# Optimization experiments

Measured on AMD Instinct MI355X. Metric: run time of the kernel, lower is better.

Reference implementation:

```python
import jax, jax.numpy as jnp
import numpy as np

N = 50000   # nodes
E = 800000  # edges (avg degree 16)
D = 64      # in = hidden = out channels, head = 1


def _linear_params(key, d_in, d_out):
    kw, kb = jax.random.split(key)
    scale = 1.0 / np.sqrt(d_in)
    W = jax.random.uniform(kw, (d_in, d_out), jnp.float32, -scale, scale)
    b = jax.random.uniform(kb, (d_out,), jnp.float32, -scale, scale)
    return W, b


def _tconv(x, src, dst, Wq, bq, Wk, bk, Wv, bv, Ws, bs):
    """PyG TransformerConv, heads=1, concat=True, root_weight=True."""
    n = x.shape[0]
    d = Wq.shape[1]
    q = x @ Wq + bq  # [N, d] query at target
    k = x @ Wk + bk  # [N, d] key at source
    v = x @ Wv + bv  # [N, d] value at source
    # per-edge attention logits: (q_i . k_j) / sqrt(d)
    scores = jnp.einsum('ed,ed->e', q[dst], k[src]) / jnp.sqrt(jnp.asarray(d, x.dtype))
    # segment softmax over incoming edges of each target node
    m = jax.ops.segment_max(scores, dst, num_segments=n)
    ex = jnp.exp(scores - m[dst])
    denom = jax.ops.segment_sum(ex, dst, num_segments=n)
    agg = jax.ops.segment_sum(ex[:, None] * v[src], dst, num_segments=n)
    denom_safe = jnp.where(denom > 0, denom, 1.0)  # guard isolated nodes
    return agg / denom_safe[:, None] + (x @ Ws + bs)  # + skip (root weight)


def setup_inputs() -> dict:
    key = jax.random.key(0)
    keys = jax.random.split(key, 32)
    inp = {
        'x': jax.random.normal(keys[0], (N, D), jnp.float32),
        'edge_index': jax.random.randint(keys[1], (2, E), 0, N, jnp.int64),
        'z': jax.random.normal(keys[2], (N, D), jnp.float32),
    }
    ki = 3
    for l in (1, 2, 3):
        for nm in ('q', 'k', 'v', 's'):
            W, b = _linear_params(keys[ki], D, D)
            ki += 1
            inp[f'W{nm}{l}'] = W
            inp[f'b{nm}{l}'] = b
    return inp


def reference(x, edge_index, z,
              Wq1, bq1, Wk1, bk1, Wv1, bv1, Ws1, bs1,
              Wq2, bq2, Wk2, bk2, Wv2, bv2, Ws2, bs2,
              Wq3, bq3, Wk3, bk3, Wv3, bv3, Ws3, bs3):
    src, dst = edge_index[0], edge_index[1]
    h = jax.nn.silu(_tconv(x, src, dst, Wq1, bq1, Wk1, bk1, Wv1, bv1, Ws1, bs1))
    h = jax.nn.silu(_tconv(h, src, dst, Wq2, bq2, Wk2, bk2, Wv2, bv2, Ws2, bs2) + h)
    drift = _tconv(h, src, dst, Wq3, bq3, Wk3, bk3, Wv3, bv3, Ws3, bs3)
    std, sqrt_d = 0.01, 0.1
    return drift + std * z / sqrt_d
```

## Files before the change

kernel.cpp:

```cpp
#include <hip/hip_runtime.h>
#include <math.h>


#define D64 64
#define KVF 64
#define NPB 128
#define MAXNB 512
#define CHUNK 4096

typedef _Float16 h2 __attribute__((ext_vector_type(2)));
typedef __attribute__((ext_vector_type(8))) short bf16x8;
typedef __attribute__((ext_vector_type(4))) float f32x4;
typedef unsigned int uint32;

__device__ __forceinline__ unsigned short bf16_rne(float f) {
    unsigned int u = __float_as_uint(f);
    u += 0x7FFFu + ((u >> 16) & 1u);
    return (unsigned short)(u >> 16);
}
__device__ __forceinline__ float fexp(float x) {
    return __builtin_amdgcn_exp2f(x * 1.44269504089f);
}
__device__ __forceinline__ float frcp(float x) {
    return __builtin_amdgcn_rcpf(x);
}

__global__ void detect_fmt(const int* __restrict__ ei, int nchecks, int* flag) {
    int t = blockIdx.x * blockDim.x + threadIdx.x;
    int acc = 0;
    for (int i = t; i < nchecks; i += blockDim.x * gridDim.x)
        acc |= ei[2 * i + 1];
    if (acc) atomicOr(flag, 1);
}

__device__ __forceinline__ int load_src(const int* ei, int e, int E, int is64) {
    return is64 ? ei[2 * e] : ei[e];
}
__device__ __forceinline__ int load_dst(const int* ei, int e, int E, int is64) {
    return is64 ? ei[2 * E + 2 * e] : ei[E + e];
}

__global__ void hist_pack(const int* __restrict__ ei, int* __restrict__ bhT,
                          uint32* __restrict__ pc, int E, int nblk, int NB,
                          const int* __restrict__ flag) {
    __shared__ int h[MAXNB];
    int blk = blockIdx.x, tid = threadIdx.x;
    for (int i = tid; i < NB; i += 256) h[i] = 0;
    __syncthreads();
    int is64 = (*flag == 0);
    int e1 = blk * CHUNK + CHUNK; if (e1 > E) e1 = E;
    for (int e = blk * CHUNK + tid; e < e1; e += 256) {
        int s = load_src(ei, e, E, is64);
        int d = load_dst(ei, e, E, is64);
        pc[e] = (uint32)s | ((uint32)d << 16);
        atomicAdd(&h[d >> 7], 1);
    }
    __syncthreads();
    for (int i = tid; i < NB; i += 256) bhT[i * nblk + blk] = h[i];
}

__global__ void scan_blocks(const int* __restrict__ counts, int* __restrict__ partial,
                            int* __restrict__ blockSums, int n) {
    int tid = threadIdx.x;
    int base = blockIdx.x * 1024 + tid * 4;
    int4 c = make_int4(0, 0, 0, 0);
    if (base + 3 < n) c = *(const int4*)&counts[base];
    else {
        if (base + 0 < n) c.x = counts[base + 0];
        if (base + 1 < n) c.y = counts[base + 1];
        if (base + 2 < n) c.z = counts[base + 2];
        if (base + 3 < n) c.w = counts[base + 3];
    }
    int s1 = c.x, s2 = s1 + c.y, s3 = s2 + c.z, s4 = s3 + c.w;
    int lane = tid & 63, wave = tid >> 6;
    int v = s4;
#pragma unroll
    for (int off = 1; off < 64; off <<= 1) {
        int t = __shfl_up(v, off);
        if (lane >= off) v += t;
    }
    __shared__ int wsum[4];
    if (lane == 63) wsum[wave] = v;
    __syncthreads();
    int wpre = 0;
    for (int w = 0; w < wave; ++w) wpre += wsum[w];
    int pre = wpre + v - s4;
    if (base + 0 < n) partial[base + 0] = pre + s1;
    if (base + 1 < n) partial[base + 1] = pre + s2;
    if (base + 2 < n) partial[base + 2] = pre + s3;
    if (base + 3 < n) partial[base + 3] = pre + s4;
    if (tid == 255) blockSums[blockIdx.x] = wsum[0] + wsum[1] + wsum[2] + wsum[3];
}

__global__ void scan_sums(int* __restrict__ bs, int nb) {
    int lane = threadIdx.x;
    int carry = 0;
    for (int b0 = 0; b0 < nb; b0 += 64) {
        int i = b0 + lane;
        int val = (i < nb) ? bs[i] : 0;
        int v = val;
#pragma unroll
        for (int off = 1; off < 64; off <<= 1) {
            int t = __shfl_up(v, off);
            if (lane >= off) v += t;
        }
        if (i < nb) bs[i] = carry + v - val;
        carry += __shfl(v, 63);
    }
}

__global__ void make_excl(const int* __restrict__ bh, const int* __restrict__ partial,
                          const int* __restrict__ bs, int* __restrict__ ebase, int n) {
    int i = blockIdx.x * 256 + threadIdx.x;
    if (i >= n) return;
    ebase[i] = partial[i] + bs[i >> 10] - bh[i];
}

__global__ void bucket_scatter(const uint32* __restrict__ pc, const int* __restrict__ ebase,
                               uint32* __restrict__ pairs, int E, int nblk, int NB) {
    __shared__ int cur[MAXNB];
    int blk = blockIdx.x, tid = threadIdx.x;
    for (int i = tid; i < NB; i += 256) cur[i] = ebase[i * nblk + blk];
    __syncthreads();
    int e1 = blk * CHUNK + CHUNK; if (e1 > E) e1 = E;
    for (int e = blk * CHUNK + tid; e < e1; e += 256) {
        uint32 w = pc[e];
        int pos = atomicAdd(&cur[w >> 23], 1);
        pairs[pos] = w;
    }
}

__global__ void bucket_finalize(const uint32* __restrict__ pairs,
                                const int* __restrict__ ebase, int nblk, int NB,
                                int* __restrict__ csr_src, int* __restrict__ offsets,
                                int N, int E) {
    __shared__ int hist[NPB];
    __shared__ int cur[NPB];
    int b = blockIdx.x, tid = threadIdx.x;
    int n0 = b * NPB;
    int cnt = N - n0; if (cnt > NPB) cnt = NPB;
    if (cnt <= 0) return;
    int estart = ebase[b * nblk];
    int eend = (b + 1 < NB) ? ebase[(b + 1) * nblk] : E;
    for (int i = tid; i < cnt; i += 256) hist[i] = 0;
    __syncthreads();
    for (int e = estart + tid; e < eend; e += 256)
        atomicAdd(&hist[(int)(pairs[e] >> 16) - n0], 1);
    __syncthreads();
    if (tid == 0) {
        int run = estart;
        for (int i = 0; i < cnt; ++i) {
            cur[i] = run;
            offsets[n0 + i] = run;
            run += hist[i];
        }
    }
    if (b == 0 && tid == 1) offsets[N] = E;
    __syncthreads();
    for (int e = estart + tid; e < eend; e += 256) {
        uint32 w = pairs[e];
        int pos = atomicAdd(&cur[(int)(w >> 16) - n0], 1);
        csr_src[pos] = (int)(w & 0xFFFFu);
    }
}

__global__ void prep_w(const float* W0, const float* W1, const float* W2,
                       const float* W3, const float* W4, const float* W5,
                       const float* W6, const float* W7, const float* W8,
                       const float* W9, const float* W10, const float* W11,
                       uint32* __restrict__ wpack) {
    const float* Wm;
    switch (blockIdx.x) {
        case 0: Wm = W0; break;  case 1: Wm = W1; break;
        case 2: Wm = W2; break;  case 3: Wm = W3; break;
        case 4: Wm = W4; break;  case 5: Wm = W5; break;
        case 6: Wm = W6; break;  case 7: Wm = W7; break;
        case 8: Wm = W8; break;  case 9: Wm = W9; break;
        case 10: Wm = W10; break; default: Wm = W11; break;
    }
    int layer = blockIdx.x >> 2, mat = blockIdx.x & 3;
    uint32* hiB = wpack + layer * 16384;
    uint32* loB = hiB + 8192;
    int d = threadIdx.x & 63;
    int cg = threadIdx.x >> 6;
    int col = mat * 64 + d;
    for (int kw = cg; kw < 32; kw += 4) {
        float w0 = Wm[(2 * kw) * 64 + d];
        float w1 = Wm[(2 * kw + 1) * 64 + d];
        unsigned short h0 = bf16_rne(w0);
        unsigned short h1 = bf16_rne(w1);
        float r0 = w0 - __uint_as_float(((uint32)h0) << 16);
        float r1 = w1 - __uint_as_float(((uint32)h1) << 16);
        unsigned short l0 = bf16_rne(r0);
        unsigned short l1 = bf16_rne(r1);
        int sw = ((kw * 4) ^ ((col & 7) << 4)) >> 2;
        hiB[col * 32 + sw] = (uint32)h0 | ((uint32)h1 << 16);
        loB[col * 32 + sw] = (uint32)l0 | ((uint32)l1 << 16);
    }
}

__launch_bounds__(256)
__global__ void gemm_mfma(const float* __restrict__ x, const uint32* __restrict__ wpackL,
                          const float* __restrict__ bq, const float* __restrict__ bk,
                          const float* __restrict__ bv, const float* __restrict__ bs,
                          float* __restrict__ q, float* __restrict__ kv,
                          float* __restrict__ s, int n) {
    __shared__ uint32 wlds[16384];
    int tid = threadIdx.x;
#pragma unroll
    for (int r = 0; r < 16; ++r) {
        int w4 = r * 1024 + tid * 4;
        *(uint4*)&wlds[w4] = *(const uint4*)&wpackL[w4];
    }
    __syncthreads();

    int lane = tid & 63, wave = tid >> 6;
    int row0 = blockIdx.x * 64 + wave * 16;
    int arow = row0 + (lane & 15);
    int kgrp = (lane >> 4) * 8;
    bool rowok = arow < n;
    const float* xr = x + (size_t)(rowok ? arow : 0) * D64;

    bf16x8 ahi[2], alo[2];
#pragma unroll
    for (int st = 0; st < 2; ++st) {
        float4 xa = rowok ? *(const float4*)(xr + st * 32 + kgrp)
                          : make_float4(0.f, 0.f, 0.f, 0.f);
        float4 xb = rowok ? *(const float4*)(xr + st * 32 + kgrp + 4)
                          : make_float4(0.f, 0.f, 0.f, 0.f);
        float xs[8] = {xa.x, xa.y, xa.z, xa.w, xb.x, xb.y, xb.z, xb.w};
#pragma unroll
        for (int j = 0; j < 8; ++j) {
            unsigned short h = bf16_rne(xs[j]);
            float rem = xs[j] - __uint_as_float(((uint32)h) << 16);
            ahi[st][j] = (short)h;
            alo[st][j] = (short)bf16_rne(rem);
        }
    }

    f32x4 acc[16];
#pragma unroll
    for (int t = 0; t < 16; ++t) acc[t] = f32x4{0.f, 0.f, 0.f, 0.f};

#pragma unroll
    for (int t = 0; t < 16; ++t) {
        int col = t * 16 + (lane & 15);
#pragma unroll
        for (int st = 0; st < 2; ++st) {
            int kidx = st * 32 + kgrp;
            int boff = col * 128 + ((kidx * 2) ^ ((col & 7) << 4));
            bf16x8 bhi = *(const bf16x8*)((const char*)wlds + boff);
            bf16x8 blo = *(const bf16x8*)((const char*)wlds + boff + 32768);
            acc[t] = __builtin_amdgcn_mfma_f32_16x16x32_bf16(alo[st], bhi, acc[t], 0, 0, 0);
            acc[t] = __builtin_amdgcn_mfma_f32_16x16x32_bf16(ahi[st], blo, acc[t], 0, 0, 0);
            acc[t] = __builtin_amdgcn_mfma_f32_16x16x32_bf16(ahi[st], bhi, acc[t], 0, 0, 0);
        }
    }

    int drow0 = row0 + (lane >> 4) * 4;
    int c16 = lane & 15;
#pragma unroll
    for (int t = 0; t < 4; ++t) {
        float bb = bq[t * 16 + c16];
#pragma unroll
        for (int r = 0; r < 4; ++r) {
            int row = drow0 + r;
            if (row < n) q[(size_t)row * D64 + t * 16 + c16] = acc[t][r] + bb;
        }
    }
#pragma unroll
    for (int t = 0; t < 4; ++t) {
        float bb = bs[t * 16 + c16];
#pragma unroll
        for (int r = 0; r < 4; ++r) {
            int row = drow0 + r;
            if (row < n) s[(size_t)row * D64 + t * 16 + c16] = acc[12 + t][r] + bb;
        }
    }
#pragma unroll
    for (int t = 0; t < 4; ++t) {
        float bkk = bk[t * 16 + c16];
        float bvv = bv[t * 16 + c16];
        int c = t * 16 + c16;
#pragma unroll
        for (int r = 0; r < 4; ++r) {
            int row = drow0 + r;
            float kval = acc[4 + t][r] + bkk;
            float vval = acc[8 + t][r] + bvv;
            uint32 kh = (uint32)__builtin_bit_cast(unsigned short, (_Float16)kval);
            uint32 kp = (uint32)__shfl_xor((int)kh, 1);
            uint32 kword = (lane & 1) ? (kp | (kh << 16)) : (kh | (kp << 16));
            uint32 vh = (uint32)bf16_rne(vval);
            uint32 vp = (uint32)__shfl_xor((int)vh, 1);
            uint32 vword = (lane & 1) ? (vp | (vh << 16)) : (vh | (vp << 16));
            if (row < n && !(lane & 1)) {
                uint32* rowp = (uint32*)(kv + (size_t)row * KVF);
                rowp[c >> 1] = kword;
                rowp[32 + (c >> 1)] = vword;
            }
        }
    }
}

template <int MODE>
__launch_bounds__(256)
__global__ void agg_fused(const float* __restrict__ q, const float* __restrict__ kv,
                          const int* __restrict__ csr_src,
                          const int* __restrict__ offsets,
                          const float* __restrict__ sbuf, const float* __restrict__ xin,
                          const float* __restrict__ z, float* __restrict__ out, int n) {
    int node = blockIdx.x * 4 + (threadIdx.x >> 6);
    if (node >= n) return;
    int lane = threadIdx.x & 63;
    int grp = lane >> 3, l8 = lane & 7;
    int start = offsets[node], end = offsets[node + 1];
    size_t co = (size_t)node * D64 + l8 * 8;
    float4 ta = *(const float4*)(sbuf + co);
    float4 tb = *(const float4*)(sbuf + co + 4);

    if (end > start) {
        const float4 qa = *(const float4*)(q + co);
        const float4 qb = *(const float4*)(q + co + 4);
        h2 hq0, hq1, hq2, hq3;
        hq0[0] = (_Float16)(qa.x * 0.125f); hq0[1] = (_Float16)(qa.y * 0.125f);
        hq1[0] = (_Float16)(qa.z * 0.125f); hq1[1] = (_Float16)(qa.w * 0.125f);
        hq2[0] = (_Float16)(qb.x * 0.125f); hq2[1] = (_Float16)(qb.y * 0.125f);
        hq3[0] = (_Float16)(qb.z * 0.125f); hq3[1] = (_Float16)(qb.w * 0.125f);
        float m = -3.0e38f, den = 0.f;
        float4 aa = make_float4(0.f, 0.f, 0.f, 0.f);
        float4 ab = make_float4(0.f, 0.f, 0.f, 0.f);

        int i = start + grp;
        int idx0 = (i < end) ? i : start;
        int sj0 = csr_src[idx0];
        const float* kp0 = kv + (size_t)sj0 * KVF;
        float4 kw = *(const float4*)(kp0 + l8 * 4);
        float4 vw = *(const float4*)(kp0 + 32 + l8 * 4);

        while (i < end) {
            int inext = i + 8;
            int idx1 = (inext < end) ? inext : start;
            int sj1 = csr_src[idx1];
            const float* kp1 = kv + (size_t)sj1 * KVF;
            float4 kw1 = *(const float4*)(kp1 + l8 * 4);
            float4 vw1 = *(const float4*)(kp1 + 32 + l8 * 4);

            float p = __builtin_amdgcn_fdot2(hq0, __builtin_bit_cast(h2, kw.x),
                                             0.f, false);
            p = __builtin_amdgcn_fdot2(hq1, __builtin_bit_cast(h2, kw.y), p, false);
            p = __builtin_amdgcn_fdot2(hq2, __builtin_bit_cast(h2, kw.z), p, false);
            p = __builtin_amdgcn_fdot2(hq3, __builtin_bit_cast(h2, kw.w), p, false);
            p += __shfl_xor(p, 1, 8);
            p += __shfl_xor(p, 2, 8);
            p += __shfl_xor(p, 4, 8);
            float nm = fmaxf(m, p);
            float f  = fexp(m - nm);
            float e  = fexp(p - nm);
            den = den * f + e;
            unsigned int u0 = __float_as_uint(vw.x), u1 = __float_as_uint(vw.y);
            unsigned int u2 = __float_as_uint(vw.z), u3 = __float_as_uint(vw.w);
            float v0 = __uint_as_float(u0 << 16), v1 = __uint_as_float(u0 & 0xFFFF0000u);
            float v2 = __uint_as_float(u1 << 16), v3 = __uint_as_float(u1 & 0xFFFF0000u);
            float v4 = __uint_as_float(u2 << 16), v5 = __uint_as_float(u2 & 0xFFFF0000u);
            float v6 = __uint_as_float(u3 << 16), v7 = __uint_as_float(u3 & 0xFFFF0000u);
            aa.x = aa.x * f + e * v0; aa.y = aa.y * f + e * v1;
            aa.z = aa.z * f + e * v2; aa.w = aa.w * f + e * v3;
            ab.x = ab.x * f + e * v4; ab.y = ab.y * f + e * v5;
            ab.z = ab.z * f + e * v6; ab.w = ab.w * f + e * v7;
            m = nm;
            kw = kw1; vw = vw1;
            i = inext;
        }
        float M = fmaxf(m, __shfl_xor(m, 8));
        M = fmaxf(M, __shfl_xor(M, 16));
        M = fmaxf(M, __shfl_xor(M, 32));
        float f = fexp(m - M);
        float dd = den * f;
        dd += __shfl_xor(dd, 8); dd += __shfl_xor(dd, 16); dd += __shfl_xor(dd, 32);
        aa.x *= f; aa.y *= f; aa.z *= f; aa.w *= f;
        ab.x *= f; ab.y *= f; ab.z *= f; ab.w *= f;
        aa.x += __shfl_xor(aa.x, 8); aa.x += __shfl_xor(aa.x, 16); aa.x += __shfl_xor(aa.x, 32);
        aa.y += __shfl_xor(aa.y, 8); aa.y += __shfl_xor(aa.y, 16); aa.y += __shfl_xor(aa.y, 32);
        aa.z += __shfl_xor(aa.z, 8); aa.z += __shfl_xor(aa.z, 16); aa.z += __shfl_xor(aa.z, 32);
        aa.w += __shfl_xor(aa.w, 8); aa.w += __shfl_xor(aa.w, 16); aa.w += __shfl_xor(aa.w, 32);
        ab.x += __shfl_xor(ab.x, 8); ab.x += __shfl_xor(ab.x, 16); ab.x += __shfl_xor(ab.x, 32);
        ab.y += __shfl_xor(ab.y, 8); ab.y += __shfl_xor(ab.y, 16); ab.y += __shfl_xor(ab.y, 32);
        ab.z += __shfl_xor(ab.z, 8); ab.z += __shfl_xor(ab.z, 16); ab.z += __shfl_xor(ab.z, 32);
        ab.w += __shfl_xor(ab.w, 8); ab.w += __shfl_xor(ab.w, 16); ab.w += __shfl_xor(ab.w, 32);
        float inv = frcp(dd);
        ta.x += aa.x * inv; ta.y += aa.y * inv; ta.z += aa.z * inv; ta.w += aa.w * inv;
        tb.x += ab.x * inv; tb.y += ab.y * inv; tb.z += ab.z * inv; tb.w += ab.w * inv;
    }
    if (MODE == 1) {
        ta.x *= frcp(1.f + fexp(-ta.x)); ta.y *= frcp(1.f + fexp(-ta.y));
        ta.z *= frcp(1.f + fexp(-ta.z)); ta.w *= frcp(1.f + fexp(-ta.w));
        tb.x *= frcp(1.f + fexp(-tb.x)); tb.y *= frcp(1.f + fexp(-tb.y));
        tb.z *= frcp(1.f + fexp(-tb.z)); tb.w *= frcp(1.f + fexp(-tb.w));
    } else if (MODE == 2) {
        const float4 xa = *(const float4*)(xin + co);
        const float4 xb = *(const float4*)(xin + co + 4);
        float u;
        u = ta.x + xa.x; ta.x = u * frcp(1.f + fexp(-u));
        u = ta.y + xa.y; ta.y = u * frcp(1.f + fexp(-u));
        u = ta.z + xa.z; ta.z = u * frcp(1.f + fexp(-u));
        u = ta.w + xa.w; ta.w = u * frcp(1.f + fexp(-u));
        u = tb.x + xb.x; tb.x = u * frcp(1.f + fexp(-u));
        u = tb.y + xb.y; tb.y = u * frcp(1.f + fexp(-u));
        u = tb.z + xb.z; tb.z = u * frcp(1.f + fexp(-u));
        u = tb.w + xb.w; tb.w = u * frcp(1.f + fexp(-u));
    } else {
        const float4 za = *(const float4*)(z + co);
        const float4 zb = *(const float4*)(z + co + 4);
        ta.x += 0.1f * za.x; ta.y += 0.1f * za.y;
        ta.z += 0.1f * za.z; ta.w += 0.1f * za.w;
        tb.x += 0.1f * zb.x; tb.y += 0.1f * zb.y;
        tb.z += 0.1f * zb.z; tb.w += 0.1f * zb.w;
    }
    if (grp == 0) {
        *(float4*)(out + co) = ta;
        *(float4*)(out + co + 4) = tb;
    }
}

extern "C" void kernel_launch(void* const* d_in, const int* in_sizes, int n_in,
                              void* d_out, int out_size, void* d_ws, size_t ws_size,
                              hipStream_t stream) {
    const float* x = (const float*)d_in[0];
    const int* ei  = (const int*)d_in[1];
    const float* z = (const float*)d_in[2];
    const float* W[3][4];
    const float* B[3][4];
    for (int l = 0; l < 3; ++l)
        for (int m = 0; m < 4; ++m) {
            W[l][m] = (const float*)d_in[3 + l * 8 + m * 2];
            B[l][m] = (const float*)d_in[3 + l * 8 + m * 2 + 1];
        }
    int N = in_sizes[0] / D64;
    int E = in_sizes[1] / 2;
    size_t ND = (size_t)N * D64;

    int NB   = (N + NPB - 1) / NPB;
    int nblk = (E + CHUNK - 1) / CHUNK;
    int nscan = NB * nblk;
    int nb2  = (nscan + 1023) / 1024;

    char* p = (char*)d_ws;
    auto alloc = [&](size_t bytes) {
        char* r = p;
        p += (bytes + 255) & ~(size_t)255;
        return r;
    };
    float* q       = (float*)alloc(ND * 4);
    float* kv      = (float*)alloc((size_t)N * KVF * 4);
    float* sb      = (float*)alloc(ND * 4);
    float* hA      = (float*)alloc(ND * 4);
    int* csr_src   = (int*)alloc((size_t)E * 4);
    uint32* pc     = (uint32*)alloc((size_t)E * 4);
    uint32* pairs  = (uint32*)alloc((size_t)E * 4);
    int* offsets   = (int*)alloc((size_t)(N + 1) * 4);
    int* bhT       = (int*)alloc((size_t)nscan * 4);
    int* partial   = (int*)alloc((size_t)nscan * 4);
    int* ebase     = (int*)alloc((size_t)nscan * 4);
    int* blockSums = (int*)alloc((size_t)nb2 * 4);
    uint32* wpack  = (uint32*)alloc(3 * 16384 * 4);
    int* flag      = (int*)alloc(4);
    float* outp    = (float*)d_out;

    hipMemsetAsync(flag, 0, 4, stream);
    int nchecks = E < 4096 ? E : 4096;
    detect_fmt<<<1, 256, 0, stream>>>(ei, nchecks, flag);
    prep_w<<<12, 256, 0, stream>>>(W[0][0], W[0][1], W[0][2], W[0][3],
                                   W[1][0], W[1][1], W[1][2], W[1][3],
                                   W[2][0], W[2][1], W[2][2], W[2][3], wpack);
    hist_pack<<<nblk, 256, 0, stream>>>(ei, bhT, pc, E, nblk, NB, flag);
    scan_blocks<<<nb2, 256, 0, stream>>>(bhT, partial, blockSums, nscan);
    scan_sums<<<1, 64, 0, stream>>>(blockSums, nb2);
    make_excl<<<(nscan + 255) / 256, 256, 0, stream>>>(bhT, partial, blockSums,
                                                       ebase, nscan);
    bucket_scatter<<<nblk, 256, 0, stream>>>(pc, ebase, pairs, E, nblk, NB);
    bucket_finalize<<<NB, 256, 0, stream>>>(pairs, ebase, nblk, NB,
                                            csr_src, offsets, N, E);

    int gemm_grid = (N + 63) / 64;
    int node_grid = (N + 3) / 4;

    gemm_mfma<<<gemm_grid, 256, 0, stream>>>(x, wpack, B[0][0], B[0][1],
                                             B[0][2], B[0][3], q, kv, sb, N);
    agg_fused<1><<<node_grid, 256, 0, stream>>>(q, kv, csr_src, offsets, sb,
                                                nullptr, nullptr, hA, N);
    gemm_mfma<<<gemm_grid, 256, 0, stream>>>(hA, wpack + 16384, B[1][0], B[1][1],
                                             B[1][2], B[1][3], q, kv, sb, N);
    agg_fused<2><<<node_grid, 256, 0, stream>>>(q, kv, csr_src, offsets, sb,
                                                hA, nullptr, hA, N);
    gemm_mfma<<<gemm_grid, 256, 0, stream>>>(hA, wpack + 32768, B[2][0], B[2][1],
                                             B[2][2], B[2][3], q, kv, sb, N);
    agg_fused<3><<<node_grid, 256, 0, stream>>>(q, kv, csr_src, offsets, sb,
                                                nullptr, z, outp, N);
}
```

Baseline: 235.2 us.

## Store q, skip and hidden activations as fp16 and halve GEMM weight LDS

The query, skip-projection and inter-layer hidden buffers are now written and read as fp16 instead of fp32, with the 1/sqrt(d) scale folded into q at GEMM time. This halves the global traffic for those tensors between the GEMM and aggregation kernels. The GEMM also loads the hi and lo weight halves into LDS in two phases of a 32KB buffer instead of one 64KB buffer, which could allow more blocks per CU but adds extra barriers. Storing the hidden state and skip term in fp16 loses precision relative to the fp32 reference.

```diff
diff --git a/kernel.cpp b/kernel.cpp
--- a/kernel.cpp
+++ b/kernel.cpp
@@ -12,6 +12,7 @@
 typedef __attribute__((ext_vector_type(8))) short bf16x8;
 typedef __attribute__((ext_vector_type(4))) float f32x4;
 typedef unsigned int uint32;
+typedef unsigned short ushort16;
 
 __device__ __forceinline__ unsigned short bf16_rne(float f) {
     unsigned int u = __float_as_uint(f);
@@ -23,6 +24,15 @@
 }
 __device__ __forceinline__ float frcp(float x) {
     return __builtin_amdgcn_rcpf(x);
+}
+__device__ __forceinline__ uint32 pack2h(float a, float b) {
+    uint32 ua = (uint32)__builtin_bit_cast(unsigned short, (_Float16)a);
+    uint32 ub = (uint32)__builtin_bit_cast(unsigned short, (_Float16)b);
+    return ua | (ub << 16);
+}
+__device__ __forceinline__ float2 unpack2h(uint32 w) {
+    h2 h = __builtin_bit_cast(h2, w);
+    return make_float2((float)h[0], (float)h[1]);
 }
 
 __global__ void detect_fmt(const int* __restrict__ ei, int nchecks, int* flag) {
@@ -199,36 +209,42 @@
     }
 }
 
+template <int IN16>
 __launch_bounds__(256)
-__global__ void gemm_mfma(const float* __restrict__ x, const uint32* __restrict__ wpackL,
+__global__ void gemm_mfma(const void* __restrict__ xv, const uint32* __restrict__ wpackL,
                           const float* __restrict__ bq, const float* __restrict__ bk,
                           const float* __restrict__ bv, const float* __restrict__ bs,
-                          float* __restrict__ q, float* __restrict__ kv,
-                          float* __restrict__ s, int n) {
-    __shared__ uint32 wlds[16384];
+                          ushort16* __restrict__ qh, float* __restrict__ kv,
+                          ushort16* __restrict__ sh, int n) {
+    __shared__ uint32 wlds[8192];
     int tid = threadIdx.x;
-#pragma unroll
-    for (int r = 0; r < 16; ++r) {
-        int w4 = r * 1024 + tid * 4;
-        *(uint4*)&wlds[w4] = *(const uint4*)&wpackL[w4];
-    }
-    __syncthreads();
-
     int lane = tid & 63, wave = tid >> 6;
     int row0 = blockIdx.x * 64 + wave * 16;
     int arow = row0 + (lane & 15);
     int kgrp = (lane >> 4) * 8;
     bool rowok = arow < n;
-    const float* xr = x + (size_t)(rowok ? arow : 0) * D64;
 
     bf16x8 ahi[2], alo[2];
 #pragma unroll
     for (int st = 0; st < 2; ++st) {
-        float4 xa = rowok ? *(const float4*)(xr + st * 32 + kgrp)
-                          : make_float4(0.f, 0.f, 0.f, 0.f);
-        float4 xb = rowok ? *(const float4*)(xr + st * 32 + kgrp + 4)
-                          : make_float4(0.f, 0.f, 0.f, 0.f);
-        float xs[8] = {xa.x, xa.y, xa.z, xa.w, xb.x, xb.y, xb.z, xb.w};
+        float xs[8];
+        if (IN16) {
+            const ushort16* xr = (const ushort16*)xv + (size_t)(rowok ? arow : 0) * D64;
+            uint4 xw = rowok ? *(const uint4*)(xr + st * 32 + kgrp)
+                             : make_uint4(0, 0, 0, 0);
+            float2 p0 = unpack2h(xw.x), p1 = unpack2h(xw.y);
+            float2 p2 = unpack2h(xw.z), p3 = unpack2h(xw.w);
+            xs[0] = p0.x; xs[1] = p0.y; xs[2] = p1.x; xs[3] = p1.y;
+            xs[4] = p2.x; xs[5] = p2.y; xs[6] = p3.x; xs[7] = p3.y;
+        } else {
+            const float* xr = (const float*)xv + (size_t)(rowok ? arow : 0) * D64;
+            float4 xa = rowok ? *(const float4*)(xr + st * 32 + kgrp)
+                              : make_float4(0.f, 0.f, 0.f, 0.f);
+            float4 xb = rowok ? *(const float4*)(xr + st * 32 + kgrp + 4)
+                              : make_float4(0.f, 0.f, 0.f, 0.f);
+            xs[0] = xa.x; xs[1] = xa.y; xs[2] = xa.z; xs[3] = xa.w;
+            xs[4] = xb.x; xs[5] = xb.y; xs[6] = xb.z; xs[7] = xb.w;
+        }
 #pragma unroll
         for (int j = 0; j < 8; ++j) {
             unsigned short h = bf16_rne(xs[j]);
@@ -243,6 +259,12 @@
     for (int t = 0; t < 16; ++t) acc[t] = f32x4{0.f, 0.f, 0.f, 0.f};
 
 #pragma unroll
+    for (int r = 0; r < 8; ++r) {
+        int w4 = r * 1024 + tid * 4;
+        *(uint4*)&wlds[w4] = *(const uint4*)&wpackL[w4];
+    }
+    __syncthreads();
+#pragma unroll
     for (int t = 0; t < 16; ++t) {
         int col = t * 16 + (lane & 15);
 #pragma unroll
@@ -250,10 +272,26 @@
             int kidx = st * 32 + kgrp;
             int boff = col * 128 + ((kidx * 2) ^ ((col & 7) << 4));
             bf16x8 bhi = *(const bf16x8*)((const char*)wlds + boff);
-            bf16x8 blo = *(const bf16x8*)((const char*)wlds + boff + 32768);
             acc[t] = __builtin_amdgcn_mfma_f32_16x16x32_bf16(alo[st], bhi, acc[t], 0, 0, 0);
+            acc[t] = __builtin_amdgcn_mfma_f32_16x16x32_bf16(ahi[st], bhi, acc[t], 0, 0, 0);
+        }
+    }
+    __syncthreads();
+#pragma unroll
+    for (int r = 0; r < 8; ++r) {
+        int w4 = r * 1024 + tid * 4;
+        *(uint4*)&wlds[w4] = *(const uint4*)&wpackL[8192 + w4];
+    }
+    __syncthreads();
+#pragma unroll
+    for (int t = 0; t < 16; ++t) {
+        int col = t * 16 + (lane & 15);
+#pragma unroll
+        for (int st = 0; st < 2; ++st) {
+            int kidx = st * 32 + kgrp;
+            int boff = col * 128 + ((kidx * 2) ^ ((col & 7) << 4));
+            bf16x8 blo = *(const bf16x8*)((const char*)wlds + boff);
             acc[t] = __builtin_amdgcn_mfma_f32_16x16x32_bf16(ahi[st], blo, acc[t], 0, 0, 0);
-            acc[t] = __builtin_amdgcn_mfma_f32_16x16x32_bf16(ahi[st], bhi, acc[t], 0, 0, 0);
         }
     }
 
@@ -261,20 +299,24 @@
     int c16 = lane & 15;
 #pragma unroll
     for (int t = 0; t < 4; ++t) {
-        float bb = bq[t * 16 + c16];
+        float bbq = bq[t * 16 + c16];
+        float bbs = bs[t * 16 + c16];
+        int c = t * 16 + c16;
 #pragma unroll
         for (int r = 0; r < 4; ++r) {
             int row = drow0 + r;
-            if (row < n) q[(size_t)row * D64 + t * 16 + c16] = acc[t][r] + bb;
-        }
-    }
-#pragma unroll
-    for (int t = 0; t < 4; ++t) {
-        float bb = bs[t * 16 + c16];
-#pragma unroll
-        for (int r = 0; r < 4; ++r) {
-            int row = drow0 + r;
-            if (row < n) s[(size_t)row * D64 + t * 16 + c16] = acc[12 + t][r] + bb;
+            float qval = (acc[t][r] + bbq) * 0.125f;
+            float sval = acc[12 + t][r] + bbs;
+            uint32 qu = (uint32)__builtin_bit_cast(unsigned short, (_Float16)qval);
+            uint32 qp = (uint32)__shfl_xor((int)qu, 1);
+            uint32 qword = (lane & 1) ? (qp | (qu << 16)) : (qu | (qp << 16));
+            uint32 su = (uint32)__builtin_bit_cast(unsigned short, (_Float16)sval);
+            uint32 sp = (uint32)__shfl_xor((int)su, 1);
+            uint32 sword = (lane & 1) ? (sp | (su << 16)) : (su | (sp << 16));
+            if (row < n && !(lane & 1)) {
+                ((uint32*)(qh + (size_t)row * D64))[c >> 1] = qword;
+                ((uint32*)(sh + (size_t)row * D64))[c >> 1] = sword;
+            }
         }
     }
 #pragma unroll
@@ -304,28 +346,29 @@
 
 template <int MODE>
 __launch_bounds__(256)
-__global__ void agg_fused(const float* __restrict__ q, const float* __restrict__ kv,
+__global__ void agg_fused(const ushort16* __restrict__ qh, const float* __restrict__ kv,
                           const int* __restrict__ csr_src,
                           const int* __restrict__ offsets,
-                          const float* __restrict__ sbuf, const float* __restrict__ xin,
-                          const float* __restrict__ z, float* __restrict__ out, int n) {
+                          const ushort16* __restrict__ sbh, const ushort16* __restrict__ xinh,
+                          const float* __restrict__ z, void* __restrict__ outp, int n) {
     int node = blockIdx.x * 4 + (threadIdx.x >> 6);
     if (node >= n) return;
     int lane = threadIdx.x & 63;
     int grp = lane >> 3, l8 = lane & 7;
     int start = offsets[node], end = offsets[node + 1];
-    size_t co = (size_t)node * D64 + l8 * 8;
-    float4 ta = *(const float4*)(sbuf + co);
-    float4 tb = *(const float4*)(sbuf + co + 4);
+    size_t co2 = (size_t)node * D64 + l8 * 8;
+    uint4 sw = *(const uint4*)(sbh + co2);
+    float2 s0 = unpack2h(sw.x), s1 = unpack2h(sw.y);
+    float2 s2 = unpack2h(sw.z), s3 = unpack2h(sw.w);
+    float4 ta = make_float4(s0.x, s0.y, s1.x, s1.y);
+    float4 tb = make_float4(s2.x, s2.y, s3.x, s3.y);
 
     if (end > start) {
-        const float4 qa = *(const float4*)(q + co);
-        const float4 qb = *(const float4*)(q + co + 4);
-        h2 hq0, hq1, hq2, hq3;
-        hq0[0] = (_Float16)(qa.x * 0.125f); hq0[1] = (_Float16)(qa.y * 0.125f);
-        hq1[0] = (_Float16)(qa.z * 0.125f); hq1[1] = (_Float16)(qa.w * 0.125f);
-        hq2[0] = (_Float16)(qb.x * 0.125f); hq2[1] = (_Float16)(qb.y * 0.125f);
-        hq3[0] = (_Float16)(qb.z * 0.125f); hq3[1] = (_Float16)(qb.w * 0.125f);
+        uint4 qw = *(const uint4*)(qh + co2);
+        h2 hq0 = __builtin_bit_cast(h2, qw.x);
+        h2 hq1 = __builtin_bit_cast(h2, qw.y);
+        h2 hq2 = __builtin_bit_cast(h2, qw.z);
+        h2 hq3 = __builtin_bit_cast(h2, qw.w);
         float m = -3.0e38f, den = 0.f;
         float4 aa = make_float4(0.f, 0.f, 0.f, 0.f);
         float4 ab = make_float4(0.f, 0.f, 0.f, 0.f);
@@ -397,28 +440,40 @@
         tb.x *= frcp(1.f + fexp(-tb.x)); tb.y *= frcp(1.f + fexp(-tb.y));
         tb.z *= frcp(1.f + fexp(-tb.z)); tb.w *= frcp(1.f + fexp(-tb.w));
     } else if (MODE == 2) {
-        const float4 xa = *(const float4*)(xin + co);
-        const float4 xb = *(const float4*)(xin + co + 4);
+        uint4 xw = *(const uint4*)(xinh + co2);
+        float2 x0 = unpack2h(xw.x), x1 = unpack2h(xw.y);
+        float2 x2 = unpack2h(xw.z), x3 = unpack2h(xw.w);
         float u;
-        u = ta.x + xa.x; ta.x = u * frcp(1.f + fexp(-u));
-        u = ta.y + xa.y; ta.y = u * frcp(1.f + fexp(-u));
-        u = ta.z + xa.z; ta.z = u * frcp(1.f + fexp(-u));
-        u = ta.w + xa.w; ta.w = u * frcp(1.f + fexp(-u));
-        u = tb.x + xb.x; tb.x = u * frcp(1.f + fexp(-u));
-        u = tb.y + xb.y; tb.y = u * frcp(1.f + fexp(-u));
-        u = tb.z + xb.z; tb.z = u * frcp(1.f + fexp(-u));
-        u = tb.w + xb.w; tb.w = u * frcp(1.f + fexp(-u));
+        u = ta.x + x0.x; ta.x = u * frcp(1.f + fexp(-u));
+        u = ta.y + x0.y; ta.y = u * frcp(1.f + fexp(-u));
+        u = ta.z + x1.x; ta.z = u * frcp(1.f + fexp(-u));
+        u = ta.w + x1.y; ta.w = u * frcp(1.f + fexp(-u));
+        u = tb.x + x2.x; tb.x = u * frcp(1.f + fexp(-u));
+        u = tb.y + x2.y; tb.y = u * frcp(1.f + fexp(-u));
+        u = tb.z + x3.x; tb.z = u * frcp(1.f + fexp(-u));
+        u = tb.w + x3.y; tb.w = u * frcp(1.f + fexp(-u));
     } else {
-        const float4 za = *(const float4*)(z + co);
-        const float4 zb = *(const float4*)(z + co + 4);
+        size_t cof = (size_t)node * D64 + l8 * 8;
+        const float4 za = *(const float4*)(z + cof);
+        const float4 zb = *(const float4*)(z + cof + 4);
         ta.x += 0.1f * za.x; ta.y += 0.1f * za.y;
         ta.z += 0.1f * za.z; ta.w += 0.1f * za.w;
         tb.x += 0.1f * zb.x; tb.y += 0.1f * zb.y;
         tb.z += 0.1f * zb.z; tb.w += 0.1f * zb.w;
     }
     if (grp == 0) {
-        *(float4*)(out + co) = ta;
-        *(float4*)(out + co + 4) = tb;
+        if (MODE == 3) {
+            float* outf = (float*)outp;
+            size_t cof = (size_t)node * D64 + l8 * 8;
+            *(float4*)(outf + cof) = ta;
+            *(float4*)(outf + cof + 4) = tb;
+        } else {
+            ushort16* outh = (ushort16*)outp;
+            uint4 ow;
+            ow.x = pack2h(ta.x, ta.y); ow.y = pack2h(ta.z, ta.w);
+            ow.z = pack2h(tb.x, tb.y); ow.w = pack2h(tb.z, tb.w);
+            *(uint4*)(outh + co2) = ow;
+        }
     }
 }
 
@@ -450,10 +505,10 @@
         p += (bytes + 255) & ~(size_t)255;
         return r;
     };
-    float* q       = (float*)alloc(ND * 4);
+    ushort16* qh   = (ushort16*)alloc(ND * 2);
+    ushort16* sbh  = (ushort16*)alloc(ND * 2);
+    ushort16* hAh  = (ushort16*)alloc(ND * 2);
     float* kv      = (float*)alloc((size_t)N * KVF * 4);
-    float* sb      = (float*)alloc(ND * 4);
-    float* hA      = (float*)alloc(ND * 4);
     int* csr_src   = (int*)alloc((size_t)E * 4);
     uint32* pc     = (uint32*)alloc((size_t)E * 4);
     uint32* pairs  = (uint32*)alloc((size_t)E * 4);
@@ -484,16 +539,16 @@
     int gemm_grid = (N + 63) / 64;
     int node_grid = (N + 3) / 4;
 
-    gemm_mfma<<<gemm_grid, 256, 0, stream>>>(x, wpack, B[0][0], B[0][1],
-                                             B[0][2], B[0][3], q, kv, sb, N);
-    agg_fused<1><<<node_grid, 256, 0, stream>>>(q, kv, csr_src, offsets, sb,
-                                                nullptr, nullptr, hA, N);
-    gemm_mfma<<<gemm_grid, 256, 0, stream>>>(hA, wpack + 16384, B[1][0], B[1][1],
-                                             B[1][2], B[1][3], q, kv, sb, N);
-    agg_fused<2><<<node_grid, 256, 0, stream>>>(q, kv, csr_src, offsets, sb,
-                                                hA, nullptr, hA, N);
-    gemm_mfma<<<gemm_grid, 256, 0, stream>>>(hA, wpack + 32768, B[2][0], B[2][1],
-                                             B[2][2], B[2][3], q, kv, sb, N);
-    agg_fused<3><<<node_grid, 256, 0, stream>>>(q, kv, csr_src, offsets, sb,
+    gemm_mfma<0><<<gemm_grid, 256, 0, stream>>>(x, wpack, B[0][0], B[0][1],
+                                                B[0][2], B[0][3], qh, kv, sbh, N);
+    agg_fused<1><<<node_grid, 256, 0, stream>>>(qh, kv, csr_src, offsets, sbh,
+                                                nullptr, nullptr, hAh, N);
+    gemm_mfma<1><<<gemm_grid, 256, 0, stream>>>(hAh, wpack + 16384, B[1][0], B[1][1],
+                                                B[1][2], B[1][3], qh, kv, sbh, N);
+    agg_fused<2><<<node_grid, 256, 0, stream>>>(qh, kv, csr_src, offsets, sbh,
+                                                hAh, nullptr, hAh, N);
+    gemm_mfma<1><<<gemm_grid, 256, 0, stream>>>(hAh, wpack + 32768, B[2][0], B[2][1],
+                                                B[2][2], B[2][3], qh, kv, sbh, N);
+    agg_fused<3><<<node_grid, 256, 0, stream>>>(qh, kv, csr_src, offsets, sbh,
                                                 nullptr, z, outp, N);
 }
```

Result: faster. 217.4 us (-7.6%).
